# Optimization experiments

Hardware: AMD Instinct MI355X
Metric: run time of the kernel (lower is better)

## Reference

```python
import jax, jax.numpy as jnp
import numpy as np

G, T, E, D, C = 4, 2048, 8, 1024, 2048
CAP_FACTORS = (0.25, 0.25, 0.125, 0.125, 0.0625, 0.0625, 0.0625, 0.0625)


def setup_inputs() -> dict:
    key = jax.random.key(0)
    k1, k2 = jax.random.split(key, 2)
    token_inputs = jax.random.normal(k1, (G, T, D), dtype=jnp.float32)
    # RouterWeights: Linear(dim -> num_experts), weight ~ N(0, 0.02), bias = 0
    W = jax.random.normal(k2, (E, D), dtype=jnp.float32) * 0.02
    b = jnp.zeros((E,), dtype=jnp.float32)
    return {"token_inputs": token_inputs, "W": W, "b": b,
            "num_experts": E, "expert_capacity": C}


def reference(token_inputs, W, b, num_experts, expert_capacity):
    # router logits [G, T, E] (jitter_noise = 0, no padding mask)
    logits = jnp.einsum('gtd,ed->gte', token_inputs, W) + b
    probs = jax.nn.softmax(logits, axis=-1)

    caps = [max(1, int(f * expert_capacity)) for f in CAP_FACTORS]
    tokens = token_inputs.shape[1]

    disp_parts, comb_parts = [], []
    for i, cap in enumerate(caps):  # fixed small loop over experts
        # each expert chooses its top-`cap` tokens
        gate, idx = jax.lax.top_k(probs[:, :, i], cap)        # [G, cap]
        onehot = jax.nn.one_hot(idx, tokens, dtype=jnp.int32)  # [G, cap, T]
        d = jnp.transpose(onehot, (0, 2, 1))                   # [G, T, cap]
        c = gate[:, None, :] * d.astype(probs.dtype)           # [G, T, cap]
        pad = expert_capacity - cap
        disp_parts.append(jnp.pad(d, ((0, 0), (0, 0), (0, pad))))
        comb_parts.append(jnp.pad(c, ((0, 0), (0, 0), (0, pad))))

    dispatch_mask = jnp.stack(disp_parts, axis=2)   # [G, T, E, C] int32
    combine_array = jnp.stack(comb_parts, axis=2)   # [G, T, E, C] float32

    router_z_loss = jnp.mean(jnp.square(jax.nn.log_softmax(logits, axis=-1)))
    return dispatch_mask, combine_array, router_z_loss
```

## Files before the change

kernel.cpp:

```cpp
#include <hip/hip_runtime.h>

#define GG 4
#define TT 2048
#define EE 8
#define DD 1024
#define CC 2048

static constexpr long long GTEC = (long long)GG * TT * EE * CC;

__global__ __launch_bounds__(256) void router_probs_kernel(
    const float* __restrict__ x, const float* __restrict__ W,
    const float* __restrict__ bias, float* __restrict__ probs,
    float* __restrict__ zloss)
{
    __shared__ float sW[EE * DD];
    __shared__ float zpart[4];
    for (int i = threadIdx.x; i < EE * DD; i += 256) sW[i] = W[i];
    __syncthreads();

    const int wave = threadIdx.x >> 6;
    const int lane = threadIdx.x & 63;
    const int token = blockIdx.x * 4 + wave;
    const float* xr = x + (long long)token * DD;

    float acc[EE];
#pragma unroll
    for (int e = 0; e < EE; ++e) acc[e] = 0.f;

#pragma unroll 4
    for (int k = lane; k < DD; k += 64) {
        float xv = xr[k];
#pragma unroll
        for (int e = 0; e < EE; ++e)
            acc[e] = fmaf(xv, sW[e * DD + k], acc[e]);
    }

#pragma unroll
    for (int off = 32; off > 0; off >>= 1) {
#pragma unroll
        for (int e = 0; e < EE; ++e)
            acc[e] += __shfl_xor(acc[e], off, 64);
    }

#pragma unroll
    for (int e = 0; e < EE; ++e) acc[e] += bias[e];

    float m = acc[0];
#pragma unroll
    for (int e = 1; e < EE; ++e) m = fmaxf(m, acc[e]);
    float s = 0.f;
#pragma unroll
    for (int e = 0; e < EE; ++e) s += expf(acc[e] - m);
    float lse = m + logf(s);

    if (lane < EE)
        probs[(long long)token * EE + lane] = expf(acc[lane] - lse);

    if (lane == 0) {
        float zs = 0.f;
#pragma unroll
        for (int e = 0; e < EE; ++e) {
            float d = acc[e] - lse;
            zs = fmaf(d, d, zs);
        }
        zpart[wave] = zs;
    }
    __syncthreads();
    if (threadIdx.x == 0) {
        float zb = (zpart[0] + zpart[1]) + (zpart[2] + zpart[3]);
        atomicAdd(zloss, zb * (1.0f / ((float)GG * TT * EE)));
    }
}

__global__ __launch_bounds__(1024) void topk_scatter_kernel(
    const float* __restrict__ probs, float* __restrict__ out)
{
    __shared__ unsigned long long keys[TT];
    const int g = blockIdx.x >> 3;
    const int e = blockIdx.x & 7;
    const int caps[EE] = {512, 512, 256, 256, 128, 128, 128, 128};
    const int cap = caps[e];

    for (int t = threadIdx.x; t < TT; t += 1024) {
        float p = probs[((long long)g * TT + t) * EE + e];
        unsigned int pb = __float_as_uint(p);
        keys[t] = ((unsigned long long)pb << 32) |
                  (unsigned long long)(0xFFFFFFFFu - (unsigned)t);
    }
    __syncthreads();

    for (int k = 2; k <= TT; k <<= 1) {
        for (int j = k >> 1; j > 0; j >>= 1) {
            for (int v = threadIdx.x; v < TT; v += 1024) {
                int ixj = v ^ j;
                if (ixj > v) {
                    bool desc = ((v & k) == 0);
                    unsigned long long a = keys[v];
                    unsigned long long b = keys[ixj];
                    bool sw = desc ? (a < b) : (a > b);
                    if (sw) { keys[v] = b; keys[ixj] = a; }
                }
            }
            __syncthreads();
        }
    }

    if (threadIdx.x < cap) {
        unsigned long long kk = keys[threadIdx.x];
        int t = (int)(0xFFFFFFFFu - (unsigned)(kk & 0xFFFFFFFFull));
        float gate = __uint_as_float((unsigned)(kk >> 32));
        long long base = (((long long)g * TT + t) * EE + e) * CC + threadIdx.x;
        out[base] = 1.0f;
        out[GTEC + base] = gate;
    }
}

extern "C" void kernel_launch(void* const* d_in, const int* in_sizes, int n_in,
                              void* d_out, int out_size, void* d_ws, size_t ws_size,
                              hipStream_t stream) {
    const float* x    = (const float*)d_in[0];
    const float* W    = (const float*)d_in[1];
    const float* bias = (const float*)d_in[2];
    float* out   = (float*)d_out;
    float* probs = (float*)d_ws;

    hipMemsetAsync(d_out, 0, (size_t)out_size * sizeof(float), stream);

    router_probs_kernel<<<GG * TT / 4, 256, 0, stream>>>(
        x, W, bias, probs, out + 2 * GTEC);

    topk_scatter_kernel<<<GG * EE, 1024, 0, stream>>>(probs, out);
}
```

Baseline: 1.094 ms.

## Replace full-output memset plus scatter with a single dense fill kernel

The large hipMemsetAsync over the whole output is dropped. The top-k kernel now records, for each token, the capacity slot it was selected into and its gate in a small workspace table. A new kernel then writes every output row once with float4 stores, placing the 1.0 and the gate directly in their slots. This removes the separate memset pass and the scattered stores that followed it, at the cost of an extra kernel launch and a per-row workspace lookup.

```diff
diff --git a/kernel.cpp b/kernel.cpp
--- a/kernel.cpp
+++ b/kernel.cpp
@@ -7,11 +7,17 @@
 #define CC 2048
 
 static constexpr long long GTEC = (long long)GG * TT * EE * CC;
+static constexpr int NROW = GG * TT * EE;
+
+static constexpr int WS_PROBS = 0;
+static constexpr int WS_SELC  = 65536;
+static constexpr int WS_SELG  = 131072;
+static constexpr int WS_ZACC  = 196608;
 
 __global__ __launch_bounds__(256) void router_probs_kernel(
     const float* __restrict__ x, const float* __restrict__ W,
     const float* __restrict__ bias, float* __restrict__ probs,
-    float* __restrict__ zloss)
+    float* __restrict__ zacc)
 {
     __shared__ float sW[EE * DD];
     __shared__ float zpart[4];
@@ -68,18 +74,20 @@
     __syncthreads();
     if (threadIdx.x == 0) {
         float zb = (zpart[0] + zpart[1]) + (zpart[2] + zpart[3]);
-        atomicAdd(zloss, zb * (1.0f / ((float)GG * TT * EE)));
+        atomicAdd(zacc, zb * (1.0f / ((float)GG * TT * EE)));
     }
 }
 
-__global__ __launch_bounds__(1024) void topk_scatter_kernel(
-    const float* __restrict__ probs, float* __restrict__ out)
+__global__ __launch_bounds__(1024) void topk_select_kernel(
+    const float* __restrict__ probs, int* __restrict__ selc,
+    float* __restrict__ selg)
 {
     __shared__ unsigned long long keys[TT];
     const int g = blockIdx.x >> 3;
     const int e = blockIdx.x & 7;
     const int caps[EE] = {512, 512, 256, 256, 128, 128, 128, 128};
     const int cap = caps[e];
+    const int base = (g * EE + e) * TT;
 
     for (int t = threadIdx.x; t < TT; t += 1024) {
         float p = probs[((long long)g * TT + t) * EE + e];
@@ -105,14 +113,52 @@
         }
     }
 
+    for (int t = threadIdx.x; t < TT; t += 1024) selc[base + t] = 0;
+    __syncthreads();
+
     if (threadIdx.x < cap) {
         unsigned long long kk = keys[threadIdx.x];
         int t = (int)(0xFFFFFFFFu - (unsigned)(kk & 0xFFFFFFFFull));
         float gate = __uint_as_float((unsigned)(kk >> 32));
-        long long base = (((long long)g * TT + t) * EE + e) * CC + threadIdx.x;
-        out[base] = 1.0f;
-        out[GTEC + base] = gate;
+        selc[base + t] = threadIdx.x + 1;
+        selg[base + t] = gate;
     }
+}
+
+__global__ __launch_bounds__(256) void fill_outputs_kernel(
+    const int* __restrict__ selc, const float* __restrict__ selg,
+    const float* __restrict__ zacc, float* __restrict__ out)
+{
+    const int wid  = (int)((blockIdx.x * 256 + threadIdx.x) >> 6);
+    const int lane = threadIdx.x & 63;
+
+    const int e = wid & (EE - 1);
+    const int t = (wid >> 3) & (TT - 1);
+    const int g = wid >> 14;
+    const int s = (g * EE + e) * TT + t;
+
+    const int   c1   = selc[s];
+    const float gate = selg[s];
+    const int   cq   = (c1 - 1) >> 2;
+    const int   cr   = (c1 - 1) & 3;
+
+    float4* drow = (float4*)out + (long long)wid * (CC / 4);
+    float4* crow = (float4*)(out + GTEC) + (long long)wid * (CC / 4);
+
+#pragma unroll
+    for (int j0 = 0; j0 < CC / 4; j0 += 64) {
+        const int j = j0 + lane;
+        float4 vd = make_float4(0.f, 0.f, 0.f, 0.f);
+        float4 vc = make_float4(0.f, 0.f, 0.f, 0.f);
+        if (c1 && j == cq) {
+            ((float*)&vd)[cr] = 1.0f;
+            ((float*)&vc)[cr] = gate;
+        }
+        drow[j] = vd;
+        crow[j] = vc;
+    }
+
+    if (wid == 0 && lane == 0) out[2 * GTEC] = zacc[0];
 }
 
 extern "C" void kernel_launch(void* const* d_in, const int* in_sizes, int n_in,
@@ -122,12 +168,19 @@
     const float* W    = (const float*)d_in[1];
     const float* bias = (const float*)d_in[2];
     float* out   = (float*)d_out;
-    float* probs = (float*)d_ws;
+    float* ws    = (float*)d_ws;
 
-    hipMemsetAsync(d_out, 0, (size_t)out_size * sizeof(float), stream);
+    float* probs = ws + WS_PROBS;
+    int*   selc  = (int*)(ws + WS_SELC);
+    float* selg  = ws + WS_SELG;
+    float* zacc  = ws + WS_ZACC;
+
+    hipMemsetAsync(zacc, 0, sizeof(float), stream);
 
     router_probs_kernel<<<GG * TT / 4, 256, 0, stream>>>(
-        x, W, bias, probs, out + 2 * GTEC);
+        x, W, bias, probs, zacc);
 
-    topk_scatter_kernel<<<GG * EE, 1024, 0, stream>>>(probs, out);
+    topk_select_kernel<<<GG * EE, 1024, 0, stream>>>(probs, selc, selg);
+
+    fill_outputs_kernel<<<NROW / 4, 256, 0, stream>>>(selc, selg, zacc, out);
 }
```

New measurement: 1.126 ms. 1.03x slower.

## Replace output memset and scatter with a single fused zero-fill kernel

Applied to the files above, without the earlier changes.

Drops the full-output hipMemsetAsync followed by a scattered write of ones and gates. Top-k selection now writes a per-token rank and gate record to workspace, and a new kernel writes every dispatch and combine row once with nontemporal vector stores, placing the nonzero value in-line. The z-loss is reduced from per-block partials instead of a global atomicAdd, and the router matvec uses float4 loads. It adds an extra kernel launch and a sel buffer read, but the output is written in one pass instead of two.

```diff
diff --git a/kernel.cpp b/kernel.cpp
--- a/kernel.cpp
+++ b/kernel.cpp
@@ -7,32 +7,51 @@
 #define CC 2048
 
 static constexpr long long GTEC = (long long)GG * TT * EE * CC;
+static constexpr int NROW = GG * TT * EE;
+static constexpr int NBLK_A = GG * TT / 4;
+
+typedef float vf4 __attribute__((ext_vector_type(4)));
+
+static constexpr int WS_PROBS = 0;
+static constexpr int WS_SEL   = 65536;
+static constexpr int WS_ZPART = 196608;
 
 __global__ __launch_bounds__(256) void router_probs_kernel(
     const float* __restrict__ x, const float* __restrict__ W,
     const float* __restrict__ bias, float* __restrict__ probs,
-    float* __restrict__ zloss)
+    float* __restrict__ zpart)
 {
     __shared__ float sW[EE * DD];
-    __shared__ float zpart[4];
-    for (int i = threadIdx.x; i < EE * DD; i += 256) sW[i] = W[i];
+    __shared__ float zsh[4];
+    {
+        const vf4* W4 = (const vf4*)W;
+        vf4* sW4 = (vf4*)sW;
+        for (int i = threadIdx.x; i < EE * DD / 4; i += 256) sW4[i] = W4[i];
+    }
     __syncthreads();
 
     const int wave = threadIdx.x >> 6;
     const int lane = threadIdx.x & 63;
     const int token = blockIdx.x * 4 + wave;
-    const float* xr = x + (long long)token * DD;
+    const vf4* xr4 = (const vf4*)(x + (long long)token * DD);
+    const vf4* sW4 = (const vf4*)sW;
 
     float acc[EE];
 #pragma unroll
     for (int e = 0; e < EE; ++e) acc[e] = 0.f;
 
-#pragma unroll 4
-    for (int k = lane; k < DD; k += 64) {
-        float xv = xr[k];
 #pragma unroll
-        for (int e = 0; e < EE; ++e)
-            acc[e] = fmaf(xv, sW[e * DD + k], acc[e]);
+    for (int it = 0; it < 4; ++it) {
+        const int k4 = lane + 64 * it;
+        const vf4 xv = xr4[k4];
+#pragma unroll
+        for (int e = 0; e < EE; ++e) {
+            const vf4 wv = sW4[e * (DD / 4) + k4];
+            acc[e] = fmaf(xv.x, wv.x, acc[e]);
+            acc[e] = fmaf(xv.y, wv.y, acc[e]);
+            acc[e] = fmaf(xv.z, wv.z, acc[e]);
+            acc[e] = fmaf(xv.w, wv.w, acc[e]);
+        }
     }
 
 #pragma unroll
@@ -51,7 +70,7 @@
     float s = 0.f;
 #pragma unroll
     for (int e = 0; e < EE; ++e) s += expf(acc[e] - m);
-    float lse = m + logf(s);
+    const float lse = m + logf(s);
 
     if (lane < EE)
         probs[(long long)token * EE + lane] = expf(acc[lane] - lse);
@@ -60,30 +79,29 @@
         float zs = 0.f;
 #pragma unroll
         for (int e = 0; e < EE; ++e) {
-            float d = acc[e] - lse;
+            const float d = acc[e] - lse;
             zs = fmaf(d, d, zs);
         }
-        zpart[wave] = zs;
+        zsh[wave] = zs;
     }
     __syncthreads();
-    if (threadIdx.x == 0) {
-        float zb = (zpart[0] + zpart[1]) + (zpart[2] + zpart[3]);
-        atomicAdd(zloss, zb * (1.0f / ((float)GG * TT * EE)));
-    }
+    if (threadIdx.x == 0)
+        zpart[blockIdx.x] = (zsh[0] + zsh[1]) + (zsh[2] + zsh[3]);
 }
 
-__global__ __launch_bounds__(1024) void topk_scatter_kernel(
-    const float* __restrict__ probs, float* __restrict__ out)
+__global__ __launch_bounds__(1024) void topk_select_kernel(
+    const float* __restrict__ probs, unsigned long long* __restrict__ sel)
 {
     __shared__ unsigned long long keys[TT];
     const int g = blockIdx.x >> 3;
     const int e = blockIdx.x & 7;
     const int caps[EE] = {512, 512, 256, 256, 128, 128, 128, 128};
     const int cap = caps[e];
+    const int base = (g * EE + e) * TT;
 
     for (int t = threadIdx.x; t < TT; t += 1024) {
-        float p = probs[((long long)g * TT + t) * EE + e];
-        unsigned int pb = __float_as_uint(p);
+        const float p = probs[((long long)g * TT + t) * EE + e];
+        const unsigned int pb = __float_as_uint(p);
         keys[t] = ((unsigned long long)pb << 32) |
                   (unsigned long long)(0xFFFFFFFFu - (unsigned)t);
     }
@@ -92,26 +110,68 @@
     for (int k = 2; k <= TT; k <<= 1) {
         for (int j = k >> 1; j > 0; j >>= 1) {
             for (int v = threadIdx.x; v < TT; v += 1024) {
-                int ixj = v ^ j;
+                const int ixj = v ^ j;
                 if (ixj > v) {
-                    bool desc = ((v & k) == 0);
-                    unsigned long long a = keys[v];
-                    unsigned long long b = keys[ixj];
-                    bool sw = desc ? (a < b) : (a > b);
-                    if (sw) { keys[v] = b; keys[ixj] = a; }
+                    const bool desc = ((v & k) == 0);
+                    const unsigned long long a = keys[v];
+                    const unsigned long long b = keys[ixj];
+                    if (desc ? (a < b) : (a > b)) { keys[v] = b; keys[ixj] = a; }
                 }
             }
             __syncthreads();
         }
     }
 
-    if (threadIdx.x < cap) {
-        unsigned long long kk = keys[threadIdx.x];
-        int t = (int)(0xFFFFFFFFu - (unsigned)(kk & 0xFFFFFFFFull));
-        float gate = __uint_as_float((unsigned)(kk >> 32));
-        long long base = (((long long)g * TT + t) * EE + e) * CC + threadIdx.x;
-        out[base] = 1.0f;
-        out[GTEC + base] = gate;
+    for (int i = threadIdx.x; i < TT; i += 1024) {
+        const unsigned long long kk = keys[i];
+        const int t = (int)(0xFFFFFFFFu - (unsigned)(kk & 0xFFFFFFFFull));
+        const unsigned int pb = (unsigned int)(kk >> 32);
+        const unsigned int rank1 = (i < cap) ? (unsigned int)(i + 1) : 0u;
+        sel[base + t] = ((unsigned long long)pb << 32) | (unsigned long long)rank1;
+    }
+}
+
+__global__ __launch_bounds__(256) void fill_outputs_kernel(
+    const unsigned long long* __restrict__ sel,
+    const float* __restrict__ zpart, float* __restrict__ out)
+{
+    const int wid  = (int)((blockIdx.x * 256 + threadIdx.x) >> 6);
+    const int lane = threadIdx.x & 63;
+
+    const int e = wid & (EE - 1);
+    const int t = (wid >> 3) & (TT - 1);
+    const int g = wid >> 14;
+
+    const unsigned long long sv = sel[(g * EE + e) * TT + t];
+    const unsigned int rank1 = (unsigned int)(sv & 0xFFFFFFFFull);
+    const float gate = __uint_as_float((unsigned int)(sv >> 32));
+    const int cq = ((int)rank1 - 1) >> 2;
+    const int cr = ((int)rank1 - 1) & 3;
+
+    vf4* drow = (vf4*)out + (long long)wid * (CC / 4);
+    vf4* crow = (vf4*)(out + GTEC) + (long long)wid * (CC / 4);
+
+#pragma unroll
+    for (int j0 = 0; j0 < CC / 4; j0 += 64) {
+        const int j = j0 + lane;
+        vf4 vd = (vf4)(0.f);
+        vf4 vc = (vf4)(0.f);
+        if (rank1 && j == cq) {
+            vd[cr] = 1.0f;
+            vc[cr] = gate;
+        }
+        __builtin_nontemporal_store(vd, &drow[j]);
+        __builtin_nontemporal_store(vc, &crow[j]);
+    }
+
+    if (blockIdx.x == 0 && threadIdx.x < 64) {
+        float zs = 0.f;
+        for (int i = lane; i < NBLK_A; i += 64) zs += zpart[i];
+#pragma unroll
+        for (int off = 32; off > 0; off >>= 1)
+            zs += __shfl_xor(zs, off, 64);
+        if (lane == 0)
+            out[2 * GTEC] = zs * (1.0f / ((float)GG * TT * EE));
     }
 }
 
@@ -121,13 +181,14 @@
     const float* x    = (const float*)d_in[0];
     const float* W    = (const float*)d_in[1];
     const float* bias = (const float*)d_in[2];
-    float* out   = (float*)d_out;
-    float* probs = (float*)d_ws;
+    float* out = (float*)d_out;
+    float* ws  = (float*)d_ws;
 
-    hipMemsetAsync(d_out, 0, (size_t)out_size * sizeof(float), stream);
+    float* probs = ws + WS_PROBS;
+    unsigned long long* sel = (unsigned long long*)(ws + WS_SEL);
+    float* zpart = ws + WS_ZPART;
 
-    router_probs_kernel<<<GG * TT / 4, 256, 0, stream>>>(
-        x, W, bias, probs, out + 2 * GTEC);
-
-    topk_scatter_kernel<<<GG * EE, 1024, 0, stream>>>(probs, out);
+    router_probs_kernel<<<NBLK_A, 256, 0, stream>>>(x, W, bias, probs, zpart);
+    topk_select_kernel<<<GG * EE, 1024, 0, stream>>>(probs, sel);
+    fill_outputs_kernel<<<NROW / 4, 256, 0, stream>>>(sel, zpart, out);
 }
```

New measurement: 1.119 ms. 1.02x slower.
